# Kernel tuning notes

Measured on AMD Instinct MI355X. Metric: run time of the kernel, lower is better.

Reference implementation:

```python
import jax, jax.numpy as jnp
import numpy as np

EPS = 1e-15
N_NODES = 20000
N_EDGES = 640000
FEAT = 128
N_RBF = 20
CUTOFF = 5.0


def setup_inputs() -> dict:
    key = jax.random.key(0)
    ks = jax.random.split(key, 10)
    s_j = jax.random.normal(ks[0], (N_NODES, FEAT), jnp.float32)
    v_j = jax.random.normal(ks[1], (N_NODES, FEAT, 3), jnp.float32)
    r_ij = jax.random.normal(ks[2], (N_EDGES, 3), jnp.float32)
    nbrs = jax.random.randint(ks[3], (N_EDGES, 2), 0, N_NODES, jnp.int64)
    # InvariantDense: Dense(F->F, swish) then Dense(F->3F)
    W1 = jax.random.normal(ks[4], (FEAT, FEAT), jnp.float32) / np.sqrt(FEAT)
    b1 = jnp.zeros((FEAT,), jnp.float32)
    W2 = jax.random.normal(ks[5], (FEAT, 3 * FEAT), jnp.float32) / np.sqrt(FEAT)
    b2 = jnp.zeros((3 * FEAT,), jnp.float32)
    # DistanceEmbed dense: Dense(n_rbf -> 3F)
    Wd = jax.random.normal(ks[6], (N_RBF, 3 * FEAT), jnp.float32) / np.sqrt(N_RBF)
    bd = jnp.zeros((3 * FEAT,), jnp.float32)
    return {"s_j": s_j, "v_j": v_j, "r_ij": r_ij, "nbrs": nbrs,
            "W1": W1, "b1": b1, "W2": W2, "b2": b2, "Wd": Wd, "bd": bd}


def reference(s_j, v_j, r_ij, nbrs, W1, b1, W2, b2, Wd, bd):
    N, F = s_j.shape
    # preprocess_r
    dist = jnp.sqrt(jnp.sum(r_ij ** 2 + EPS, axis=-1))          # [E]
    unit = r_ij / dist[:, None]                                  # [E,3]
    # InvariantDense on nodes (dense before gather, as in torch code)
    phi_node = jax.nn.silu(s_j @ W1 + b1) @ W2 + b2              # [N,3F]
    phi = phi_node[nbrs[:, 1]]                                   # [E,3F]
    # PaiNN radial basis: sin(n*pi*d/cutoff)/d, n=1..n_rbf
    k = jnp.arange(1, N_RBF + 1, dtype=dist.dtype) * (np.pi / CUTOFF)  # [n_rbf]
    rbf = jnp.sin(dist[:, None] * k[None, :]) / dist[:, None]    # [E,n_rbf]
    # cosine cutoff envelope
    env = 0.5 * (jnp.cos(np.pi * dist / CUTOFF) + 1.0)
    env = jnp.where(dist < CUTOFF, env, 0.0)                     # [E]
    w_s = (rbf @ Wd + bd) * env[:, None]                         # [E,3F]
    inv = (phi * w_s).reshape(-1, 3, F)                          # [E,3,F]
    split0 = inv[:, 0, :][:, :, None]                            # [E,F,1]
    split1 = inv[:, 1, :]                                        # [E,F]
    split2 = inv[:, 2, :][:, :, None]                            # [E,F,1]
    delta_v_ij = split2 * unit[:, None, :] + split0 * v_j[nbrs[:, 1]]  # [E,F,3]
    idx = nbrs[:, 0]
    delta_s_i = jax.ops.segment_sum(split1, idx, num_segments=N)      # [N,F]
    delta_v_i = jax.ops.segment_sum(delta_v_ij, idx, num_segments=N)  # [N,F,3]
    return (delta_s_i, delta_v_i)
```

## Files before the change

kernel.cpp:

```cpp
#include <hip/hip_runtime.h>
#include <hip/hip_bf16.h>
#include <math.h>

typedef __hip_bfloat16 bf16;

#define FEAT 128
#define NRBF 20
#define CUTOFF_F 5.0f

__device__ __forceinline__ float b2f(bf16 x) { return __bfloat162float(x); }
__device__ __forceinline__ bf16 f2b(float x) { return __float2bfloat16(x); }

template<int F32>
__device__ __forceinline__ float LD(const void* p, size_t i) {
    if (F32) return ((const float*)p)[i];
    return b2f(((const bf16*)p)[i]);
}
template<int F32>
__device__ __forceinline__ void ST(void* p, size_t i, float v) {
    if (F32) ((float*)p)[i] = v;
    else ((bf16*)p)[i] = f2b(v);
}

__device__ __forceinline__ int get_dst(const int* nb, int e, int is64) {
    return is64 ? nb[4 * e] : nb[2 * e];
}
__device__ __forceinline__ int get_src(const int* nb, int e, int is64) {
    return is64 ? nb[4 * e + 2] : nb[2 * e + 1];
}
__device__ __forceinline__ int clampi(int v, int n) {
    return v < 0 ? 0 : (v >= n ? n - 1 : v);
}

__global__ void init_kernel(const void* __restrict__ s_ptr, const int* __restrict__ nbrs32,
                            int nE, int* __restrict__ flags, int* __restrict__ counts, int nN) {
    int t = blockIdx.x * blockDim.x + threadIdx.x;
    if (t < nN) counts[t] = 0;
    if (t == 0) {
        const unsigned* u = (const unsigned*)s_ptr;
        int hits = 0;
        for (int i = 0; i < 64; ++i) {
            unsigned ef = (u[i] >> 7) & 0xFF;
            hits += (ef >= 110 && ef <= 135) ? 1 : 0;
        }
        flags[0] = (hits < 32) ? 1 : 0;
        int lim = 2 * nE; if (lim > 128) lim = 128;
        int allz = 1;
        for (int i = 1; i < lim; i += 2) allz &= (nbrs32[i] == 0);
        flags[1] = allz;
    }
}

__global__ void hist_kernel(const int* __restrict__ nbrs, const int* __restrict__ flags,
                            int* __restrict__ counts, int nE, int nN) {
    int e = blockIdx.x * blockDim.x + threadIdx.x;
    if (e < nE) {
        int d = clampi(get_dst(nbrs, e, flags[1]), nN);
        atomicAdd(&counts[d], 1);
    }
}

__global__ __launch_bounds__(1024) void scan_kernel(const int* __restrict__ counts,
        int* __restrict__ offsets, int* __restrict__ cursor, int nN) {
    __shared__ int part[1024];
    const int t = threadIdx.x;
    const int chunk = (nN + 1023) / 1024;
    const int base = t * chunk;
    int local[32];
    int sum = 0;
    for (int c = 0; c < chunk && c < 32; ++c) {
        int idx = base + c;
        int v = (idx < nN) ? counts[idx] : 0;
        local[c] = v;
        sum += v;
    }
    part[t] = sum;
    __syncthreads();
    for (int off = 1; off < 1024; off <<= 1) {
        int add = (t >= off) ? part[t - off] : 0;
        __syncthreads();
        part[t] += add;
        __syncthreads();
    }
    int run = part[t] - sum;
    for (int c = 0; c < chunk && c < 32; ++c) {
        int idx = base + c;
        if (idx < nN) { offsets[idx] = run; cursor[idx] = run; run += local[c]; }
    }
    if (t == 1023) offsets[nN] = part[1023];
}

__global__ void scatter_kernel(const int* __restrict__ nbrs, const int* __restrict__ flags,
                               int* __restrict__ cursor, int* __restrict__ edge_ids,
                               int nE, int nN) {
    int e = blockIdx.x * blockDim.x + threadIdx.x;
    if (e < nE) {
        int d = clampi(get_dst(nbrs, e, flags[1]), nN);
        int pos = atomicAdd(&cursor[d], 1);
        if (pos >= 0 && pos < nE) edge_ids[pos] = e;
    }
}

template<int F32, int PHIM>
__device__ void gemm_body(const void* __restrict__ s_j, const void* __restrict__ W1,
                          const void* __restrict__ b1, const void* __restrict__ W2,
                          const void* __restrict__ b2v, void* __restrict__ phi, int nN) {
    __shared__ float sl[8][FEAT];
    __shared__ float hl[8][FEAT];
    const int t = threadIdx.x;
    const int n0 = blockIdx.x * 8;
    for (int idx = t; idx < 8 * FEAT; idx += 384) {
        int n = idx >> 7, k = idx & 127;
        int row = n0 + n;
        sl[n][k] = (row < nN) ? LD<F32>(s_j, (size_t)row * FEAT + k) : 0.f;
    }
    __syncthreads();
    if (t < FEAT) {
        float acc[8] = {};
        #pragma unroll 4
        for (int k = 0; k < FEAT; ++k) {
            const float w = LD<F32>(W1, (size_t)k * FEAT + t);
            #pragma unroll
            for (int n = 0; n < 8; ++n) acc[n] = fmaf(sl[n][k], w, acc[n]);
        }
        const float bb = LD<F32>(b1, t);
        #pragma unroll
        for (int n = 0; n < 8; ++n) {
            float xv = acc[n] + bb;
            float sg = F32 ? (1.0f / (1.0f + expf(-xv))) : (1.0f / (1.0f + __expf(-xv)));
            hl[n][t] = xv * sg;
        }
    }
    __syncthreads();
    float acc[8] = {};
    #pragma unroll 4
    for (int k = 0; k < FEAT; ++k) {
        const float w = LD<F32>(W2, (size_t)k * 384 + t);
        #pragma unroll
        for (int n = 0; n < 8; ++n) acc[n] = fmaf(hl[n][k], w, acc[n]);
    }
    const float bb = LD<F32>(b2v, t);
    #pragma unroll
    for (int n = 0; n < 8; ++n) {
        int row = n0 + n;
        if (row < nN) ST<PHIM>(phi, (size_t)row * 384 + t, acc[n] + bb);
    }
}

template<int PHIM>
__global__ __launch_bounds__(384) void gemm_node_kernel(const void* s_j, const void* W1,
        const void* b1, const void* W2, const void* b2v, void* phi,
        const int* __restrict__ flags, int nN) {
    if (flags[0]) gemm_body<1, PHIM>(s_j, W1, b1, W2, b2v, phi, nN);
    else          gemm_body<0, PHIM>(s_j, W1, b1, W2, b2v, phi, nN);
}

template<int F32, int PHIM>
__device__ void msg_body(const int* __restrict__ nbrs, int is64,
        const void* __restrict__ r_ij, const void* __restrict__ v_j,
        const void* __restrict__ Wd, const void* __restrict__ bd,
        const void* __restrict__ phi,
        const int* __restrict__ offsets, const int* __restrict__ edge_ids,
        void* __restrict__ out, int nE, int nN) {
    const int i = blockIdx.x;
    const int f = threadIdx.x;

    float wd0[NRBF], wd1[NRBF], wd2[NRBF];
    #pragma unroll
    for (int k = 0; k < NRBF; ++k) {
        wd0[k] = LD<F32>(Wd, (size_t)k * 384 + f);
        wd1[k] = LD<F32>(Wd, (size_t)k * 384 + FEAT + f);
        wd2[k] = LD<F32>(Wd, (size_t)k * 384 + 2 * FEAT + f);
    }
    const float bd0 = LD<F32>(bd, f);
    const float bd1 = LD<F32>(bd, FEAT + f);
    const float bd2 = LD<F32>(bd, 2 * FEAT + f);

    float ds = 0.f, dv0 = 0.f, dv1 = 0.f, dv2 = 0.f;

    int start = offsets[i];
    int end   = offsets[i + 1];
    if (start < 0) start = 0;
    if (end > nE) end = nE;
    const float kscale = 0.62831853071795864769f;

    for (int p = start; p < end; ++p) {
        const int e = clampi(edge_ids[p], nE);
        const int j = clampi(get_src(nbrs, e, is64), nN);
        const float rx = LD<F32>(r_ij, (size_t)3 * e + 0);
        const float ry = LD<F32>(r_ij, (size_t)3 * e + 1);
        const float rz = LD<F32>(r_ij, (size_t)3 * e + 2);
        const float d2   = rx * rx + ry * ry + rz * rz + 3e-15f;
        const float invd = rsqrtf(d2);
        const float d    = d2 * invd;
        const float ux = rx * invd, uy = ry * invd, uz = rz * invd;
        const float x  = d * kscale;
        const float s1 = F32 ? sinf(x) : __sinf(x);
        const float c1 = F32 ? cosf(x) : __cosf(x);
        const float env = (d < CUTOFF_F) ? (0.5f * (c1 + 1.0f)) : 0.0f;
        const float tc = 2.0f * c1;
        float skm2 = 0.f, skm1 = s1;
        float t0 = s1 * wd0[0], t1 = s1 * wd1[0], t2 = s1 * wd2[0];
        #pragma unroll
        for (int k = 1; k < NRBF; ++k) {
            const float sk = fmaf(tc, skm1, -skm2);
            t0 = fmaf(sk, wd0[k], t0);
            t1 = fmaf(sk, wd1[k], t1);
            t2 = fmaf(sk, wd2[k], t2);
            skm2 = skm1; skm1 = sk;
        }
        const float w0 = fmaf(t0, invd, bd0) * env;
        const float w1 = fmaf(t1, invd, bd1) * env;
        const float w2 = fmaf(t2, invd, bd2) * env;

        const size_t pb = (size_t)j * 384;
        const float p0 = LD<PHIM>(phi, pb + f);
        const float p1 = LD<PHIM>(phi, pb + FEAT + f);
        const float p2 = LD<PHIM>(phi, pb + 2 * FEAT + f);
        const size_t vb = ((size_t)j * FEAT + f) * 3;
        const float vx = LD<F32>(v_j, vb + 0);
        const float vy = LD<F32>(v_j, vb + 1);
        const float vz = LD<F32>(v_j, vb + 2);

        const float i0 = w0 * p0;
        const float i1 = w1 * p1;
        const float i2 = w2 * p2;
        ds += i1;
        dv0 = fmaf(i2, ux, fmaf(i0, vx, dv0));
        dv1 = fmaf(i2, uy, fmaf(i0, vy, dv1));
        dv2 = fmaf(i2, uz, fmaf(i0, vz, dv2));
    }

    ST<F32>(out, (size_t)i * FEAT + f, ds);
    const size_t ob = (size_t)nN * FEAT + ((size_t)i * FEAT + f) * 3;
    ST<F32>(out, ob + 0, dv0);
    ST<F32>(out, ob + 1, dv1);
    ST<F32>(out, ob + 2, dv2);
}

template<int PHIM>
__global__ __launch_bounds__(128) void msg_kernel(const int* nbrs,
        const void* r_ij, const void* v_j, const void* Wd, const void* bd,
        const void* phi, const int* __restrict__ flags,
        const int* offsets, const int* edge_ids, void* out, int nE, int nN) {
    if (flags[0]) msg_body<1, PHIM>(nbrs, flags[1], r_ij, v_j, Wd, bd, phi, offsets, edge_ids, out, nE, nN);
    else          msg_body<0, PHIM>(nbrs, flags[1], r_ij, v_j, Wd, bd, phi, offsets, edge_ids, out, nE, nN);
}

extern "C" void kernel_launch(void* const* d_in, const int* in_sizes, int n_in,
                              void* d_out, int out_size, void* d_ws, size_t ws_size,
                              hipStream_t stream) {
    const void* s_j  = d_in[0];
    const void* v_j  = d_in[1];
    const void* r_ij = d_in[2];
    const int*  nbrs = (const int*)d_in[3];
    const void* W1   = d_in[4];
    const void* b1   = d_in[5];
    const void* W2   = d_in[6];
    const void* b2   = d_in[7];
    const void* Wd   = d_in[8];
    const void* bd   = d_in[9];

    const int nN = out_size / (4 * FEAT);
    const int nE = in_sizes[2] / 3;

    char* ws = (char*)d_ws;
    size_t off = 0;
    int* flags = (int*)(ws + off);    off += 256;
    int* counts = (int*)(ws + off);   off += ((size_t)nN * 4 + 255) & ~(size_t)255;
    int* offsets = (int*)(ws + off);  off += (((size_t)nN + 1) * 4 + 255) & ~(size_t)255;
    int* cursor = (int*)(ws + off);   off += ((size_t)nN * 4 + 255) & ~(size_t)255;
    int* edge_ids = (int*)(ws + off); off += ((size_t)nE * 4 + 255) & ~(size_t)255;
    void* phi = (void*)(ws + off);
    const size_t phi_f32_bytes = (size_t)nN * 384 * 4;
    const int phim = (ws_size >= off + phi_f32_bytes) ? 1 : 0;

    init_kernel<<<(nN + 255) / 256, 256, 0, stream>>>(s_j, nbrs, nE, flags, counts, nN);
    if (phim)
        gemm_node_kernel<1><<<(nN + 7) / 8, 384, 0, stream>>>(s_j, W1, b1, W2, b2, phi, flags, nN);
    else
        gemm_node_kernel<0><<<(nN + 7) / 8, 384, 0, stream>>>(s_j, W1, b1, W2, b2, phi, flags, nN);
    hist_kernel<<<(nE + 255) / 256, 256, 0, stream>>>(nbrs, flags, counts, nE, nN);
    scan_kernel<<<1, 1024, 0, stream>>>(counts, offsets, cursor, nN);
    scatter_kernel<<<(nE + 255) / 256, 256, 0, stream>>>(nbrs, flags, cursor, edge_ids, nE, nN);
    if (phim)
        msg_kernel<1><<<nN, 128, 0, stream>>>(nbrs, r_ij, v_j, Wd, bd, phi, flags,
                                              offsets, edge_ids, d_out, nE, nN);
    else
        msg_kernel<0><<<nN, 128, 0, stream>>>(nbrs, r_ij, v_j, Wd, bd, phi, flags,
                                              offsets, edge_ids, d_out, nE, nN);
}
```

Before: 608.4 us.

## Precompute per-edge radial basis into workspace and store phi as bf16

Adds a per-edge pre-pass that computes the scaled sine basis, unit vector and envelope once per edge and stores them in a workspace buffer (fp32 or bf16 depending on space), instead of recomputing them in every feature thread of the message kernel. It also stores the node phi table in bf16, uniformizes edge/source indices with readfirstlane, spreads the first GEMM stage over all 384 threads, and launches both dtype variants of the kernels, which exit early on a device flag. The cost is an extra edge-sized buffer to write and read, extra empty kernel launches, and reduced precision of phi.

```diff
diff --git a/kernel.cpp b/kernel.cpp
--- a/kernel.cpp
+++ b/kernel.cpp
@@ -7,6 +7,7 @@
 #define FEAT 128
 #define NRBF 20
 #define CUTOFF_F 5.0f
+#define KSCALE 0.62831853071795864769f
 
 __device__ __forceinline__ float b2f(bf16 x) { return __bfloat162float(x); }
 __device__ __forceinline__ bf16 f2b(float x) { return __float2bfloat16(x); }
@@ -101,10 +102,49 @@
     }
 }
 
-template<int F32, int PHIM>
+template<int F32, int GM>
+__global__ __launch_bounds__(256) void pre_kernel(const void* __restrict__ r_ij,
+        void* __restrict__ gbuf, const int* __restrict__ flags, int nE) {
+    if (flags[0] != F32) return;
+    int e = blockIdx.x * blockDim.x + threadIdx.x;
+    if (e >= nE) return;
+    const float rx = LD<F32>(r_ij, (size_t)3 * e + 0);
+    const float ry = LD<F32>(r_ij, (size_t)3 * e + 1);
+    const float rz = LD<F32>(r_ij, (size_t)3 * e + 2);
+    const float d2   = rx * rx + ry * ry + rz * rz + 3e-15f;
+    const float invd = rsqrtf(d2);
+    const float d    = d2 * invd;
+    const float x  = d * KSCALE;
+    const float s1 = F32 ? sinf(x) : __sinf(x);
+    const float c1 = F32 ? cosf(x) : __cosf(x);
+    const float env = (d < CUTOFF_F) ? (0.5f * (c1 + 1.0f)) : 0.0f;
+    const float scale = invd * env;
+    float rec[24];
+    const float tc = 2.0f * c1;
+    float skm2 = 0.f, skm1 = s1;
+    rec[0] = s1 * scale;
+    #pragma unroll
+    for (int k = 1; k < NRBF; ++k) {
+        const float sk = fmaf(tc, skm1, -skm2);
+        rec[k] = sk * scale;
+        skm2 = skm1; skm1 = sk;
+    }
+    rec[20] = rx * invd; rec[21] = ry * invd; rec[22] = rz * invd; rec[23] = env;
+    if (GM == 2) {
+        float* dst = (float*)gbuf + (size_t)24 * e;
+        #pragma unroll
+        for (int i = 0; i < 24; ++i) dst[i] = rec[i];
+    } else {
+        bf16* dst = (bf16*)gbuf + (size_t)24 * e;
+        #pragma unroll
+        for (int i = 0; i < 24; ++i) dst[i] = f2b(rec[i]);
+    }
+}
+
+template<int F32>
 __device__ void gemm_body(const void* __restrict__ s_j, const void* __restrict__ W1,
                           const void* __restrict__ b1, const void* __restrict__ W2,
-                          const void* __restrict__ b2v, void* __restrict__ phi, int nN) {
+                          const void* __restrict__ b2v, bf16* __restrict__ phi, int nN) {
     __shared__ float sl[8][FEAT];
     __shared__ float hl[8][FEAT];
     const int t = threadIdx.x;
@@ -115,21 +155,14 @@
         sl[n][k] = (row < nN) ? LD<F32>(s_j, (size_t)row * FEAT + k) : 0.f;
     }
     __syncthreads();
-    if (t < FEAT) {
-        float acc[8] = {};
+    for (int idx = t; idx < 8 * FEAT; idx += 384) {
+        int n = idx >> 7, f = idx & 127;
+        float a = 0.f;
         #pragma unroll 4
-        for (int k = 0; k < FEAT; ++k) {
-            const float w = LD<F32>(W1, (size_t)k * FEAT + t);
-            #pragma unroll
-            for (int n = 0; n < 8; ++n) acc[n] = fmaf(sl[n][k], w, acc[n]);
-        }
-        const float bb = LD<F32>(b1, t);
-        #pragma unroll
-        for (int n = 0; n < 8; ++n) {
-            float xv = acc[n] + bb;
-            float sg = F32 ? (1.0f / (1.0f + expf(-xv))) : (1.0f / (1.0f + __expf(-xv)));
-            hl[n][t] = xv * sg;
-        }
+        for (int k = 0; k < FEAT; ++k) a = fmaf(sl[n][k], LD<F32>(W1, (size_t)k * FEAT + f), a);
+        a += LD<F32>(b1, f);
+        float sg = F32 ? (1.0f / (1.0f + expf(-a))) : (1.0f / (1.0f + __expf(-a)));
+        hl[n][f] = a * sg;
     }
     __syncthreads();
     float acc[8] = {};
@@ -143,27 +176,29 @@
     #pragma unroll
     for (int n = 0; n < 8; ++n) {
         int row = n0 + n;
-        if (row < nN) ST<PHIM>(phi, (size_t)row * 384 + t, acc[n] + bb);
-    }
-}
-
-template<int PHIM>
+        if (row < nN) phi[(size_t)row * 384 + t] = f2b(acc[n] + bb);
+    }
+}
+
 __global__ __launch_bounds__(384) void gemm_node_kernel(const void* s_j, const void* W1,
-        const void* b1, const void* W2, const void* b2v, void* phi,
+        const void* b1, const void* W2, const void* b2v, bf16* phi,
         const int* __restrict__ flags, int nN) {
-    if (flags[0]) gemm_body<1, PHIM>(s_j, W1, b1, W2, b2v, phi, nN);
-    else          gemm_body<0, PHIM>(s_j, W1, b1, W2, b2v, phi, nN);
-}
-
-template<int F32, int PHIM>
-__device__ void msg_body(const int* __restrict__ nbrs, int is64,
-        const void* __restrict__ r_ij, const void* __restrict__ v_j,
-        const void* __restrict__ Wd, const void* __restrict__ bd,
-        const void* __restrict__ phi,
+    if (flags[0]) gemm_body<1>(s_j, W1, b1, W2, b2v, phi, nN);
+    else          gemm_body<0>(s_j, W1, b1, W2, b2v, phi, nN);
+}
+
+template<int F32, int GM>
+__global__ __launch_bounds__(128, 2) void msg_kernel(
+        const int* __restrict__ nbrs, const void* __restrict__ r_ij,
+        const void* __restrict__ v_j, const void* __restrict__ Wd,
+        const void* __restrict__ bd, const bf16* __restrict__ phi,
+        const void* __restrict__ gbuf, const int* __restrict__ flags,
         const int* __restrict__ offsets, const int* __restrict__ edge_ids,
         void* __restrict__ out, int nE, int nN) {
+    if (flags[0] != F32) return;
     const int i = blockIdx.x;
     const int f = threadIdx.x;
+    const int is64 = flags[1];
 
     float wd0[NRBF], wd1[NRBF], wd2[NRBF];
     #pragma unroll
@@ -182,41 +217,60 @@
     int end   = offsets[i + 1];
     if (start < 0) start = 0;
     if (end > nE) end = nE;
-    const float kscale = 0.62831853071795864769f;
 
     for (int p = start; p < end; ++p) {
-        const int e = clampi(edge_ids[p], nE);
-        const int j = clampi(get_src(nbrs, e, is64), nN);
-        const float rx = LD<F32>(r_ij, (size_t)3 * e + 0);
-        const float ry = LD<F32>(r_ij, (size_t)3 * e + 1);
-        const float rz = LD<F32>(r_ij, (size_t)3 * e + 2);
-        const float d2   = rx * rx + ry * ry + rz * rz + 3e-15f;
-        const float invd = rsqrtf(d2);
-        const float d    = d2 * invd;
-        const float ux = rx * invd, uy = ry * invd, uz = rz * invd;
-        const float x  = d * kscale;
-        const float s1 = F32 ? sinf(x) : __sinf(x);
-        const float c1 = F32 ? cosf(x) : __cosf(x);
-        const float env = (d < CUTOFF_F) ? (0.5f * (c1 + 1.0f)) : 0.0f;
-        const float tc = 2.0f * c1;
-        float skm2 = 0.f, skm1 = s1;
-        float t0 = s1 * wd0[0], t1 = s1 * wd1[0], t2 = s1 * wd2[0];
+        const int e = __builtin_amdgcn_readfirstlane(clampi(edge_ids[p], nE));
+        const int j = __builtin_amdgcn_readfirstlane(clampi(get_src(nbrs, e, is64), nN));
+
+        float gk[24];
+        if (GM == 2) {
+            const float* g = (const float*)gbuf + (size_t)24 * e;
+            #pragma unroll
+            for (int q = 0; q < 24; ++q) gk[q] = g[q];
+        } else if (GM == 1) {
+            const bf16* g = (const bf16*)gbuf + (size_t)24 * e;
+            #pragma unroll
+            for (int q = 0; q < 24; ++q) gk[q] = b2f(g[q]);
+        } else {
+            const float rx = LD<F32>(r_ij, (size_t)3 * e + 0);
+            const float ry = LD<F32>(r_ij, (size_t)3 * e + 1);
+            const float rz = LD<F32>(r_ij, (size_t)3 * e + 2);
+            const float d2   = rx * rx + ry * ry + rz * rz + 3e-15f;
+            const float invd = rsqrtf(d2);
+            const float d    = d2 * invd;
+            const float x  = d * KSCALE;
+            const float s1 = F32 ? sinf(x) : __sinf(x);
+            const float c1 = F32 ? cosf(x) : __cosf(x);
+            const float env = (d < CUTOFF_F) ? (0.5f * (c1 + 1.0f)) : 0.0f;
+            const float scale = invd * env;
+            const float tc = 2.0f * c1;
+            float skm2 = 0.f, skm1 = s1;
+            gk[0] = s1 * scale;
+            #pragma unroll
+            for (int k = 1; k < NRBF; ++k) {
+                const float sk = fmaf(tc, skm1, -skm2);
+                gk[k] = sk * scale;
+                skm2 = skm1; skm1 = sk;
+            }
+            gk[20] = rx * invd; gk[21] = ry * invd; gk[22] = rz * invd; gk[23] = env;
+        }
+
+        float t0 = 0.f, t1 = 0.f, t2 = 0.f;
         #pragma unroll
-        for (int k = 1; k < NRBF; ++k) {
-            const float sk = fmaf(tc, skm1, -skm2);
-            t0 = fmaf(sk, wd0[k], t0);
-            t1 = fmaf(sk, wd1[k], t1);
-            t2 = fmaf(sk, wd2[k], t2);
-            skm2 = skm1; skm1 = sk;
+        for (int k = 0; k < NRBF; ++k) {
+            t0 = fmaf(gk[k], wd0[k], t0);
+            t1 = fmaf(gk[k], wd1[k], t1);
+            t2 = fmaf(gk[k], wd2[k], t2);
         }
-        const float w0 = fmaf(t0, invd, bd0) * env;
-        const float w1 = fmaf(t1, invd, bd1) * env;
-        const float w2 = fmaf(t2, invd, bd2) * env;
+        const float env = gk[23];
+        const float w0 = fmaf(bd0, env, t0);
+        const float w1 = fmaf(bd1, env, t1);
+        const float w2 = fmaf(bd2, env, t2);
 
         const size_t pb = (size_t)j * 384;
-        const float p0 = LD<PHIM>(phi, pb + f);
-        const float p1 = LD<PHIM>(phi, pb + FEAT + f);
-        const float p2 = LD<PHIM>(phi, pb + 2 * FEAT + f);
+        const float p0 = b2f(phi[pb + f]);
+        const float p1 = b2f(phi[pb + FEAT + f]);
+        const float p2 = b2f(phi[pb + 2 * FEAT + f]);
         const size_t vb = ((size_t)j * FEAT + f) * 3;
         const float vx = LD<F32>(v_j, vb + 0);
         const float vy = LD<F32>(v_j, vb + 1);
@@ -226,9 +280,9 @@
         const float i1 = w1 * p1;
         const float i2 = w2 * p2;
         ds += i1;
-        dv0 = fmaf(i2, ux, fmaf(i0, vx, dv0));
-        dv1 = fmaf(i2, uy, fmaf(i0, vy, dv1));
-        dv2 = fmaf(i2, uz, fmaf(i0, vz, dv2));
+        dv0 = fmaf(i2, gk[20], fmaf(i0, vx, dv0));
+        dv1 = fmaf(i2, gk[21], fmaf(i0, vy, dv1));
+        dv2 = fmaf(i2, gk[22], fmaf(i0, vz, dv2));
     }
 
     ST<F32>(out, (size_t)i * FEAT + f, ds);
@@ -236,15 +290,6 @@
     ST<F32>(out, ob + 0, dv0);
     ST<F32>(out, ob + 1, dv1);
     ST<F32>(out, ob + 2, dv2);
-}
-
-template<int PHIM>
-__global__ __launch_bounds__(128) void msg_kernel(const int* nbrs,
-        const void* r_ij, const void* v_j, const void* Wd, const void* bd,
-        const void* phi, const int* __restrict__ flags,
-        const int* offsets, const int* edge_ids, void* out, int nE, int nN) {
-    if (flags[0]) msg_body<1, PHIM>(nbrs, flags[1], r_ij, v_j, Wd, bd, phi, offsets, edge_ids, out, nE, nN);
-    else          msg_body<0, PHIM>(nbrs, flags[1], r_ij, v_j, Wd, bd, phi, offsets, edge_ids, out, nE, nN);
 }
 
 extern "C" void kernel_launch(void* const* d_in, const int* in_sizes, int n_in,
@@ -271,22 +316,42 @@
     int* offsets = (int*)(ws + off);  off += (((size_t)nN + 1) * 4 + 255) & ~(size_t)255;
     int* cursor = (int*)(ws + off);   off += ((size_t)nN * 4 + 255) & ~(size_t)255;
     int* edge_ids = (int*)(ws + off); off += ((size_t)nE * 4 + 255) & ~(size_t)255;
-    void* phi = (void*)(ws + off);
-    const size_t phi_f32_bytes = (size_t)nN * 384 * 4;
-    const int phim = (ws_size >= off + phi_f32_bytes) ? 1 : 0;
+
+    const size_t phi_bytes = (size_t)nN * 384 * sizeof(bf16);
+    const size_t g32_bytes = (size_t)nE * 24 * 4;
+    const size_t g16_bytes = (size_t)nE * 24 * 2;
+    int GM;
+    size_t g_bytes;
+    if (ws_size >= off + g32_bytes + phi_bytes)      { GM = 2; g_bytes = g32_bytes; }
+    else if (ws_size >= off + g16_bytes + phi_bytes) { GM = 1; g_bytes = g16_bytes; }
+    else                                             { GM = 0; g_bytes = 0; }
+    void* gbuf = (void*)(ws + off);   off += (g_bytes + 255) & ~(size_t)255;
+    bf16* phi = (bf16*)(ws + off);
 
     init_kernel<<<(nN + 255) / 256, 256, 0, stream>>>(s_j, nbrs, nE, flags, counts, nN);
-    if (phim)
-        gemm_node_kernel<1><<<(nN + 7) / 8, 384, 0, stream>>>(s_j, W1, b1, W2, b2, phi, flags, nN);
-    else
-        gemm_node_kernel<0><<<(nN + 7) / 8, 384, 0, stream>>>(s_j, W1, b1, W2, b2, phi, flags, nN);
+
+    const int preg = (nE + 255) / 256;
+    if (GM == 2) {
+        pre_kernel<0, 2><<<preg, 256, 0, stream>>>(r_ij, gbuf, flags, nE);
+        pre_kernel<1, 2><<<preg, 256, 0, stream>>>(r_ij, gbuf, flags, nE);
+    } else if (GM == 1) {
+        pre_kernel<0, 1><<<preg, 256, 0, stream>>>(r_ij, gbuf, flags, nE);
+        pre_kernel<1, 1><<<preg, 256, 0, stream>>>(r_ij, gbuf, flags, nE);
+    }
+
+    gemm_node_kernel<<<(nN + 7) / 8, 384, 0, stream>>>(s_j, W1, b1, W2, b2, phi, flags, nN);
     hist_kernel<<<(nE + 255) / 256, 256, 0, stream>>>(nbrs, flags, counts, nE, nN);
     scan_kernel<<<1, 1024, 0, stream>>>(counts, offsets, cursor, nN);
     scatter_kernel<<<(nE + 255) / 256, 256, 0, stream>>>(nbrs, flags, cursor, edge_ids, nE, nN);
-    if (phim)
-        msg_kernel<1><<<nN, 128, 0, stream>>>(nbrs, r_ij, v_j, Wd, bd, phi, flags,
-                                              offsets, edge_ids, d_out, nE, nN);
-    else
-        msg_kernel<0><<<nN, 128, 0, stream>>>(nbrs, r_ij, v_j, Wd, bd, phi, flags,
-                                              offsets, edge_ids, d_out, nE, nN);
-}
+
+    if (GM == 2) {
+        msg_kernel<0, 2><<<nN, 128, 0, stream>>>(nbrs, r_ij, v_j, Wd, bd, phi, gbuf, flags, offsets, edge_ids, d_out, nE, nN);
+        msg_kernel<1, 2><<<nN, 128, 0, stream>>>(nbrs, r_ij, v_j, Wd, bd, phi, gbuf, flags, offsets, edge_ids, d_out, nE, nN);
+    } else if (GM == 1) {
+        msg_kernel<0, 1><<<nN, 128, 0, stream>>>(nbrs, r_ij, v_j, Wd, bd, phi, gbuf, flags, offsets, edge_ids, d_out, nE, nN);
+        msg_kernel<1, 1><<<nN, 128, 0, stream>>>(nbrs, r_ij, v_j, Wd, bd, phi, gbuf, flags, offsets, edge_ids, d_out, nE, nN);
+    } else {
+        msg_kernel<0, 0><<<nN, 128, 0, stream>>>(nbrs, r_ij, v_j, Wd, bd, phi, gbuf, flags, offsets, edge_ids, d_out, nE, nN);
+        msg_kernel<1, 0><<<nN, 128, 0, stream>>>(nbrs, r_ij, v_j, Wd, bd, phi, gbuf, flags, offsets, edge_ids, d_out, nE, nN);
+    }
+}
```

Result: faster. 596.2 us (-2.0%).

## Precompute per-edge RBF/envelope in scatter pass; split message kernel into 384-thread channel groups

Applied to the files above, without the earlier changes.

Per-edge geometry (unit vector, envelope, and the RBF basis scaled by envelope/d) is now computed once in the scatter kernel and written to workspace, instead of being recomputed by all 128 threads of each destination block. The message kernel uses 384 threads, one per output channel of the 3F split, with a transposed Wd held in registers. Each channel group accumulates its own piece, and the two vector parts are combined through shared memory. phi is stored in bf16 to halve gather traffic. This adds about 70 B of per-edge workspace writes and reads plus reduced precision on phi, and each thread reads the 20-float g row per edge.

```diff
diff --git a/kernel.cpp b/kernel.cpp
--- a/kernel.cpp
+++ b/kernel.cpp
@@ -7,6 +7,7 @@
 #define FEAT 128
 #define NRBF 20
 #define CUTOFF_F 5.0f
+#define KSCALE 0.62831853071795864769f
 
 __device__ __forceinline__ float b2f(bf16 x) { return __bfloat162float(x); }
 __device__ __forceinline__ bf16 f2b(float x) { return __float2bfloat16(x); }
@@ -90,21 +91,69 @@
     if (t == 1023) offsets[nN] = part[1023];
 }
 
-__global__ void scatter_kernel(const int* __restrict__ nbrs, const int* __restrict__ flags,
-                               int* __restrict__ cursor, int* __restrict__ edge_ids,
-                               int nE, int nN) {
+__global__ __launch_bounds__(384) void prep_kernel(const void* __restrict__ Wd,
+        const void* __restrict__ bd, float* __restrict__ WdT, float* __restrict__ bdT,
+        const int* __restrict__ flags) {
+    const int c = threadIdx.x;
+    if (flags[0]) {
+        for (int k = 0; k < NRBF; ++k) WdT[c * NRBF + k] = ((const float*)Wd)[k * 384 + c];
+        bdT[c] = ((const float*)bd)[c];
+    } else {
+        for (int k = 0; k < NRBF; ++k) WdT[c * NRBF + k] = b2f(((const bf16*)Wd)[k * 384 + c]);
+        bdT[c] = b2f(((const bf16*)bd)[c]);
+    }
+}
+
+template<int F32>
+__device__ void pre_scatter_body(const void* __restrict__ r_ij, const int* __restrict__ nbrs,
+        int is64, int* __restrict__ cursor, int* __restrict__ edge_ids,
+        int* __restrict__ src_e, float4* __restrict__ u_env_e, float* __restrict__ g_e,
+        int e, int nE, int nN) {
+    const int d = clampi(get_dst(nbrs, e, is64), nN);
+    const int j = clampi(get_src(nbrs, e, is64), nN);
+    int pos = atomicAdd(&cursor[d], 1);
+    pos = clampi(pos, nE);
+    edge_ids[pos] = e;
+    src_e[e] = j;
+
+    const float rx = LD<F32>(r_ij, (size_t)3 * e + 0);
+    const float ry = LD<F32>(r_ij, (size_t)3 * e + 1);
+    const float rz = LD<F32>(r_ij, (size_t)3 * e + 2);
+    const float d2   = rx * rx + ry * ry + rz * rz + 3e-15f;
+    const float invd = rsqrtf(d2);
+    const float dd   = d2 * invd;
+    const float x  = dd * KSCALE;
+    const float s1 = F32 ? sinf(x) : __sinf(x);
+    const float c1 = F32 ? cosf(x) : __cosf(x);
+    const float env = (dd < CUTOFF_F) ? (0.5f * (c1 + 1.0f)) : 0.0f;
+    u_env_e[e] = make_float4(rx * invd, ry * invd, rz * invd, env);
+
+    const float scale = invd * env;
+    const float tc = 2.0f * c1;
+    float skm2 = 0.f, skm1 = s1;
+    float* g = g_e + (size_t)e * NRBF;
+    g[0] = s1 * scale;
+    #pragma unroll
+    for (int k = 1; k < NRBF; ++k) {
+        const float sk = fmaf(tc, skm1, -skm2);
+        g[k] = sk * scale;
+        skm2 = skm1; skm1 = sk;
+    }
+}
+
+__global__ __launch_bounds__(256) void pre_scatter_kernel(const void* r_ij, const int* nbrs,
+        const int* __restrict__ flags, int* cursor, int* edge_ids, int* src_e,
+        float4* u_env_e, float* g_e, int nE, int nN) {
     int e = blockIdx.x * blockDim.x + threadIdx.x;
-    if (e < nE) {
-        int d = clampi(get_dst(nbrs, e, flags[1]), nN);
-        int pos = atomicAdd(&cursor[d], 1);
-        if (pos >= 0 && pos < nE) edge_ids[pos] = e;
-    }
-}
-
-template<int F32, int PHIM>
+    if (e >= nE) return;
+    if (flags[0]) pre_scatter_body<1>(r_ij, nbrs, flags[1], cursor, edge_ids, src_e, u_env_e, g_e, e, nE, nN);
+    else          pre_scatter_body<0>(r_ij, nbrs, flags[1], cursor, edge_ids, src_e, u_env_e, g_e, e, nE, nN);
+}
+
+template<int F32>
 __device__ void gemm_body(const void* __restrict__ s_j, const void* __restrict__ W1,
                           const void* __restrict__ b1, const void* __restrict__ W2,
-                          const void* __restrict__ b2v, void* __restrict__ phi, int nN) {
+                          const void* __restrict__ b2v, bf16* __restrict__ phi, int nN) {
     __shared__ float sl[8][FEAT];
     __shared__ float hl[8][FEAT];
     const int t = threadIdx.x;
@@ -115,21 +164,14 @@
         sl[n][k] = (row < nN) ? LD<F32>(s_j, (size_t)row * FEAT + k) : 0.f;
     }
     __syncthreads();
-    if (t < FEAT) {
-        float acc[8] = {};
+    for (int idx = t; idx < 8 * FEAT; idx += 384) {
+        int n = idx >> 7, f = idx & 127;
+        float a = 0.f;
         #pragma unroll 4
-        for (int k = 0; k < FEAT; ++k) {
-            const float w = LD<F32>(W1, (size_t)k * FEAT + t);
-            #pragma unroll
-            for (int n = 0; n < 8; ++n) acc[n] = fmaf(sl[n][k], w, acc[n]);
-        }
-        const float bb = LD<F32>(b1, t);
-        #pragma unroll
-        for (int n = 0; n < 8; ++n) {
-            float xv = acc[n] + bb;
-            float sg = F32 ? (1.0f / (1.0f + expf(-xv))) : (1.0f / (1.0f + __expf(-xv)));
-            hl[n][t] = xv * sg;
-        }
+        for (int k = 0; k < FEAT; ++k) a = fmaf(sl[n][k], LD<F32>(W1, (size_t)k * FEAT + f), a);
+        a += LD<F32>(b1, f);
+        float sg = F32 ? (1.0f / (1.0f + expf(-a))) : (1.0f / (1.0f + __expf(-a)));
+        hl[n][f] = a * sg;
     }
     __syncthreads();
     float acc[8] = {};
@@ -143,108 +185,90 @@
     #pragma unroll
     for (int n = 0; n < 8; ++n) {
         int row = n0 + n;
-        if (row < nN) ST<PHIM>(phi, (size_t)row * 384 + t, acc[n] + bb);
-    }
-}
-
-template<int PHIM>
+        if (row < nN) phi[(size_t)row * 384 + t] = f2b(acc[n] + bb);
+    }
+}
+
 __global__ __launch_bounds__(384) void gemm_node_kernel(const void* s_j, const void* W1,
-        const void* b1, const void* W2, const void* b2v, void* phi,
+        const void* b1, const void* W2, const void* b2v, bf16* phi,
         const int* __restrict__ flags, int nN) {
-    if (flags[0]) gemm_body<1, PHIM>(s_j, W1, b1, W2, b2v, phi, nN);
-    else          gemm_body<0, PHIM>(s_j, W1, b1, W2, b2v, phi, nN);
-}
-
-template<int F32, int PHIM>
-__device__ void msg_body(const int* __restrict__ nbrs, int is64,
-        const void* __restrict__ r_ij, const void* __restrict__ v_j,
-        const void* __restrict__ Wd, const void* __restrict__ bd,
-        const void* __restrict__ phi,
+    if (flags[0]) gemm_body<1>(s_j, W1, b1, W2, b2v, phi, nN);
+    else          gemm_body<0>(s_j, W1, b1, W2, b2v, phi, nN);
+}
+
+template<int F32>
+__device__ void msg_body(const bf16* __restrict__ phi, const void* __restrict__ v_j,
+        const float* __restrict__ WdT, const float* __restrict__ bdT,
         const int* __restrict__ offsets, const int* __restrict__ edge_ids,
-        void* __restrict__ out, int nE, int nN) {
+        const int* __restrict__ src_e, const float4* __restrict__ u_env_e,
+        const float* __restrict__ g_e, void* __restrict__ out, int nE, int nN) {
     const int i = blockIdx.x;
-    const int f = threadIdx.x;
-
-    float wd0[NRBF], wd1[NRBF], wd2[NRBF];
+    const int t = threadIdx.x;
+    const int grp = t >> 7;
+    const int f = t & 127;
+
+    float wd[NRBF];
     #pragma unroll
-    for (int k = 0; k < NRBF; ++k) {
-        wd0[k] = LD<F32>(Wd, (size_t)k * 384 + f);
-        wd1[k] = LD<F32>(Wd, (size_t)k * 384 + FEAT + f);
-        wd2[k] = LD<F32>(Wd, (size_t)k * 384 + 2 * FEAT + f);
-    }
-    const float bd0 = LD<F32>(bd, f);
-    const float bd1 = LD<F32>(bd, FEAT + f);
-    const float bd2 = LD<F32>(bd, 2 * FEAT + f);
-
-    float ds = 0.f, dv0 = 0.f, dv1 = 0.f, dv2 = 0.f;
+    for (int k = 0; k < NRBF; ++k) wd[k] = WdT[(size_t)t * NRBF + k];
+    const float bdv = bdT[t];
 
     int start = offsets[i];
     int end   = offsets[i + 1];
     if (start < 0) start = 0;
     if (end > nE) end = nE;
-    const float kscale = 0.62831853071795864769f;
-
+
+    float a0 = 0.f, a1 = 0.f, a2 = 0.f;
+
+    #pragma unroll 2
     for (int p = start; p < end; ++p) {
         const int e = clampi(edge_ids[p], nE);
-        const int j = clampi(get_src(nbrs, e, is64), nN);
-        const float rx = LD<F32>(r_ij, (size_t)3 * e + 0);
-        const float ry = LD<F32>(r_ij, (size_t)3 * e + 1);
-        const float rz = LD<F32>(r_ij, (size_t)3 * e + 2);
-        const float d2   = rx * rx + ry * ry + rz * rz + 3e-15f;
-        const float invd = rsqrtf(d2);
-        const float d    = d2 * invd;
-        const float ux = rx * invd, uy = ry * invd, uz = rz * invd;
-        const float x  = d * kscale;
-        const float s1 = F32 ? sinf(x) : __sinf(x);
-        const float c1 = F32 ? cosf(x) : __cosf(x);
-        const float env = (d < CUTOFF_F) ? (0.5f * (c1 + 1.0f)) : 0.0f;
-        const float tc = 2.0f * c1;
-        float skm2 = 0.f, skm1 = s1;
-        float t0 = s1 * wd0[0], t1 = s1 * wd1[0], t2 = s1 * wd2[0];
+        const int j = clampi(src_e[e], nN);
+        const float4 ue = u_env_e[e];
+        const float* g = g_e + (size_t)e * NRBF;
+
+        float w = bdv * ue.w;
         #pragma unroll
-        for (int k = 1; k < NRBF; ++k) {
-            const float sk = fmaf(tc, skm1, -skm2);
-            t0 = fmaf(sk, wd0[k], t0);
-            t1 = fmaf(sk, wd1[k], t1);
-            t2 = fmaf(sk, wd2[k], t2);
-            skm2 = skm1; skm1 = sk;
+        for (int k = 0; k < NRBF; ++k) w = fmaf(g[k], wd[k], w);
+
+        const float ph = b2f(phi[(size_t)j * 384 + t]);
+        const float im = w * ph;
+
+        if (grp == 0) {
+            const size_t vb = ((size_t)j * FEAT + f) * 3;
+            const float vx = LD<F32>(v_j, vb + 0);
+            const float vy = LD<F32>(v_j, vb + 1);
+            const float vz = LD<F32>(v_j, vb + 2);
+            a0 = fmaf(im, vx, a0);
+            a1 = fmaf(im, vy, a1);
+            a2 = fmaf(im, vz, a2);
+        } else if (grp == 1) {
+            a0 += im;
+        } else {
+            a0 = fmaf(im, ue.x, a0);
+            a1 = fmaf(im, ue.y, a1);
+            a2 = fmaf(im, ue.z, a2);
         }
-        const float w0 = fmaf(t0, invd, bd0) * env;
-        const float w1 = fmaf(t1, invd, bd1) * env;
-        const float w2 = fmaf(t2, invd, bd2) * env;
-
-        const size_t pb = (size_t)j * 384;
-        const float p0 = LD<PHIM>(phi, pb + f);
-        const float p1 = LD<PHIM>(phi, pb + FEAT + f);
-        const float p2 = LD<PHIM>(phi, pb + 2 * FEAT + f);
-        const size_t vb = ((size_t)j * FEAT + f) * 3;
-        const float vx = LD<F32>(v_j, vb + 0);
-        const float vy = LD<F32>(v_j, vb + 1);
-        const float vz = LD<F32>(v_j, vb + 2);
-
-        const float i0 = w0 * p0;
-        const float i1 = w1 * p1;
-        const float i2 = w2 * p2;
-        ds += i1;
-        dv0 = fmaf(i2, ux, fmaf(i0, vx, dv0));
-        dv1 = fmaf(i2, uy, fmaf(i0, vy, dv1));
-        dv2 = fmaf(i2, uz, fmaf(i0, vz, dv2));
-    }
-
-    ST<F32>(out, (size_t)i * FEAT + f, ds);
-    const size_t ob = (size_t)nN * FEAT + ((size_t)i * FEAT + f) * 3;
-    ST<F32>(out, ob + 0, dv0);
-    ST<F32>(out, ob + 1, dv1);
-    ST<F32>(out, ob + 2, dv2);
-}
-
-template<int PHIM>
-__global__ __launch_bounds__(128) void msg_kernel(const int* nbrs,
-        const void* r_ij, const void* v_j, const void* Wd, const void* bd,
-        const void* phi, const int* __restrict__ flags,
-        const int* offsets, const int* edge_ids, void* out, int nE, int nN) {
-    if (flags[0]) msg_body<1, PHIM>(nbrs, flags[1], r_ij, v_j, Wd, bd, phi, offsets, edge_ids, out, nE, nN);
-    else          msg_body<0, PHIM>(nbrs, flags[1], r_ij, v_j, Wd, bd, phi, offsets, edge_ids, out, nE, nN);
+    }
+
+    __shared__ float dc[FEAT][3];
+    if (grp == 2) { dc[f][0] = a0; dc[f][1] = a1; dc[f][2] = a2; }
+    __syncthreads();
+    if (grp == 0) {
+        const size_t ob = (size_t)nN * FEAT + ((size_t)i * FEAT + f) * 3;
+        ST<F32>(out, ob + 0, a0 + dc[f][0]);
+        ST<F32>(out, ob + 1, a1 + dc[f][1]);
+        ST<F32>(out, ob + 2, a2 + dc[f][2]);
+    } else if (grp == 1) {
+        ST<F32>(out, (size_t)i * FEAT + f, a0);
+    }
+}
+
+__global__ __launch_bounds__(384) void msg_kernel(const bf16* phi, const void* v_j,
+        const float* WdT, const float* bdT, const int* offsets, const int* edge_ids,
+        const int* src_e, const float4* u_env_e, const float* g_e,
+        const int* __restrict__ flags, void* out, int nE, int nN) {
+    if (flags[0]) msg_body<1>(phi, v_j, WdT, bdT, offsets, edge_ids, src_e, u_env_e, g_e, out, nE, nN);
+    else          msg_body<0>(phi, v_j, WdT, bdT, offsets, edge_ids, src_e, u_env_e, g_e, out, nE, nN);
 }
 
 extern "C" void kernel_launch(void* const* d_in, const int* in_sizes, int n_in,
@@ -266,27 +290,34 @@
 
     char* ws = (char*)d_ws;
     size_t off = 0;
-    int* flags = (int*)(ws + off);    off += 256;
-    int* counts = (int*)(ws + off);   off += ((size_t)nN * 4 + 255) & ~(size_t)255;
-    int* offsets = (int*)(ws + off);  off += (((size_t)nN + 1) * 4 + 255) & ~(size_t)255;
-    int* cursor = (int*)(ws + off);   off += ((size_t)nN * 4 + 255) & ~(size_t)255;
-    int* edge_ids = (int*)(ws + off); off += ((size_t)nE * 4 + 255) & ~(size_t)255;
-    void* phi = (void*)(ws + off);
-    const size_t phi_f32_bytes = (size_t)nN * 384 * 4;
-    const int phim = (ws_size >= off + phi_f32_bytes) ? 1 : 0;
+    auto alloc = [&](size_t bytes) -> void* {
+        void* p = ws + off;
+        off = (off + bytes + 255) & ~(size_t)255;
+        return p;
+    };
+    int*    flags    = (int*)alloc(16);
+    int*    counts   = (int*)alloc((size_t)nN * 4);
+    int*    offsets  = (int*)alloc(((size_t)nN + 1) * 4);
+    int*    cursor   = (int*)alloc((size_t)nN * 4);
+    int*    edge_ids = (int*)alloc((size_t)nE * 4);
+    int*    src_e    = (int*)alloc((size_t)nE * 4);
+    float4* u_env_e  = (float4*)alloc((size_t)nE * 16);
+    float*  g_e      = (float*)alloc((size_t)nE * NRBF * 4);
+    float*  WdT      = (float*)alloc((size_t)384 * NRBF * 4);
+    float*  bdT      = (float*)alloc((size_t)384 * 4);
+    bf16*   phi      = (bf16*)alloc((size_t)nN * 384 * 2);
+    (void)ws_size;
 
     init_kernel<<<(nN + 255) / 256, 256, 0, stream>>>(s_j, nbrs, nE, flags, counts, nN);
-    if (phim)
-        gemm_node_kernel<1><<<(nN + 7) / 8, 384, 0, stream>>>(s_j, W1, b1, W2, b2, phi, flags, nN);
-    else
-        gemm_node_kernel<0><<<(nN + 7) / 8, 384, 0, stream>>>(s_j, W1, b1, W2, b2, phi, flags, nN);
     hist_kernel<<<(nE + 255) / 256, 256, 0, stream>>>(nbrs, flags, counts, nE, nN);
     scan_kernel<<<1, 1024, 0, stream>>>(counts, offsets, cursor, nN);
-    scatter_kernel<<<(nE + 255) / 256, 256, 0, stream>>>(nbrs, flags, cursor, edge_ids, nE, nN);
-    if (phim)
-        msg_kernel<1><<<nN, 128, 0, stream>>>(nbrs, r_ij, v_j, Wd, bd, phi, flags,
-                                              offsets, edge_ids, d_out, nE, nN);
-    else
-        msg_kernel<0><<<nN, 128, 0, stream>>>(nbrs, r_ij, v_j, Wd, bd, phi, flags,
-                                              offsets, edge_ids, d_out, nE, nN);
-}
+    prep_kernel<<<1, 384, 0, stream>>>(Wd, bd, WdT, bdT, flags);
+
+    pre_scatter_kernel<<<(nE + 255) / 256, 256, 0, stream>>>(
+        r_ij, nbrs, flags, cursor, edge_ids, src_e, u_env_e, g_e, nE, nN);
+
+    gemm_node_kernel<<<(nN + 7) / 8, 384, 0, stream>>>(s_j, W1, b1, W2, b2, phi, flags, nN);
+
+    msg_kernel<<<nN, 384, 0, stream>>>(phi, v_j, WdT, bdT, offsets, edge_ids,
+                                       src_e, u_env_e, g_e, flags, d_out, nE, nN);
+}
```

Measured after the change: 873.9 us. 43.6% more time.
